# Kernel optimization log

Hardware: AMD Instinct MI355X
Metric: run time of the kernel (lower is better)

The kernel has to match this reference:

```python
import jax, jax.numpy as jnp
import numpy as np

WEIGHT = 1.0
TEMPERATURE = 1.0
POWER = 2.0
NEG_FILL = -1e9
EPS = 1e-8


def _cos_sim_matrix(x):
    # row-normalize then GEMM: equivalent to pairwise F.cosine_similarity
    norms = jnp.linalg.norm(x, axis=-1, keepdims=True)
    xn = x / jnp.maximum(norms, EPS)
    return xn @ xn.T  # [N, N]


def setup_inputs() -> dict:
    key = jax.random.key(0)
    k1, k2 = jax.random.split(key)
    model_output = jax.random.normal(k1, (8192, 512), dtype=jnp.float32)
    targets = jax.random.normal(k2, (8192, 768), dtype=jnp.float32)
    return {"model_output": model_output, "targets": targets}


def reference(model_output, targets):
    N = model_output.shape[0]
    eye = jnp.eye(N, dtype=bool)

    sim_o = jnp.where(eye, NEG_FILL, _cos_sim_matrix(model_output))
    sim_t = jnp.where(eye, NEG_FILL, _cos_sim_matrix(targets))

    student_log_probs = jax.nn.log_softmax(sim_o / TEMPERATURE, axis=-1)
    teacher_probs = jax.nn.softmax(sim_t / TEMPERATURE, axis=-1)

    weights = jax.lax.stop_gradient(teacher_probs ** POWER)

    # torch F.kl_div(input=log_p_student, target=p_teacher, reduction='none')
    # = where(target > 0, target * (log(target) - input), 0)
    tp_safe = jnp.where(teacher_probs > 0, teacher_probs, 1.0)
    kl = jnp.where(teacher_probs > 0,
                   teacher_probs * (jnp.log(tp_safe) - student_log_probs),
                   0.0)

    loss = jnp.mean(weights * kl)
    return WEIGHT * loss
```

## Files before the change

### kernel.cpp

```cpp
#include <hip/hip_runtime.h>

#define N    8192
#define DT   768
#define DO   512
#define BM   128
#define BN   128
#define TI   (N / BM)
#define TJ   (N / BN)
#define NTILE (TI * (TI + 1) / 2)
#define NSLOT (2 * TJ)
#define PL    ((size_t)NSLOT * N)

typedef __attribute__((ext_vector_type(8))) short   short8;
typedef __attribute__((ext_vector_type(4))) float   floatx4;

struct alignas(8) us4 { unsigned short x[4]; };

__device__ inline unsigned short f2bf(float x) {
    union { float f; unsigned int u; } v; v.f = x;
    unsigned int r = v.u + 0x7fffu + ((v.u >> 16) & 1u);
    return (unsigned short)(r >> 16);
}
__device__ inline float bf2f(unsigned short u) {
    union { unsigned int u; float f; } v; v.u = ((unsigned int)u) << 16;
    return v.f;
}

__device__ inline void gl2lds16(const unsigned short* g, unsigned short* l) {
    __builtin_amdgcn_global_load_lds(
        (const __attribute__((address_space(1))) unsigned int*)(const void*)g,
        (__attribute__((address_space(3))) unsigned int*)(void*)l,
        16, 0, 0);
}

template <int D>
__device__ inline void stage_tile(const unsigned short* __restrict__ Xi,
                                  const unsigned short* __restrict__ Xj,
                                  unsigned short* sA, unsigned short* sB,
                                  int i0, int j0, int k, int t) {
    #pragma unroll
    for (int h = 0; h < 2; ++h) {
        const int idx = t + h * 256;
        const int r   = idx >> 2;
        const int cs  = ((idx & 3) ^ ((r >> 1) & 3)) << 3;
        gl2lds16(Xi + (size_t)(i0 + r) * D + k + cs, &sA[idx * 8]);
        gl2lds16(Xj + (size_t)(j0 + r) * D + k + cs, &sB[idx * 8]);
    }
}

__global__ void norm_kernel(const float* __restrict__ Tg,
                            const float* __restrict__ Mo,
                            unsigned short* __restrict__ Xt,
                            unsigned short* __restrict__ Xo,
                            float* __restrict__ zero_me) {
    if (blockIdx.x == 0 && threadIdx.x == 0) zero_me[0] = 0.0f;
    int bid = blockIdx.x;
    const float* X; unsigned short* Xn; int D;
    if (bid < N / 4) { X = Tg; Xn = Xt; D = DT; }
    else             { bid -= N / 4; X = Mo; Xn = Xo; D = DO; }
    const int row  = bid * 4 + (threadIdx.x >> 6);
    const int lane = threadIdx.x & 63;
    const float* xr = X + (size_t)row * D;
    float ss = 0.0f;
    for (int c = lane * 4; c < D; c += 256) {
        const floatx4 v = *(const floatx4*)(xr + c);
        ss += v[0] * v[0] + v[1] * v[1] + v[2] * v[2] + v[3] * v[3];
    }
    #pragma unroll
    for (int m = 32; m >= 1; m >>= 1) ss += __shfl_xor(ss, m);
    const float scale = 1.0f / fmaxf(sqrtf(ss), 1e-8f);
    unsigned short* outr = Xn + (size_t)row * D;
    for (int c = lane * 4; c < D; c += 256) {
        const floatx4 v = *(const floatx4*)(xr + c);
        us4 o;
        #pragma unroll
        for (int j = 0; j < 4; ++j) o.x[j] = f2bf(v[j] * scale);
        *(us4*)(outr + c) = o;
    }
}

__launch_bounds__(256, 3)
__global__ void fused_kernel(const unsigned short* __restrict__ Xt,
                             const unsigned short* __restrict__ Xo,
                             float* __restrict__ partials) {
    __shared__ unsigned short sA[BM * 32];
    __shared__ unsigned short sB[BN * 32];
    __shared__ unsigned short sW[64 * 256];

    const int t    = threadIdx.x;
    const int lane = t & 63;
    const int w    = t >> 6;
    const int wm   = w >> 1, wn = w & 1;
    const int lr   = lane & 15, lg = lane >> 4;
    const int swz  = (lr >> 1) & 3;

    const int swb = (blockIdx.x & 7) * (NTILE / 8) + (blockIdx.x >> 3);
    int rem = swb, ti = 0;
    while (rem >= TI - ti) { rem -= TI - ti; ++ti; }
    const int tj = ti + rem;
    const bool offdiag = (ti != tj);
    const int i0 = ti * BM, j0 = tj * BN;

    floatx4 acc[4][4];
    #pragma unroll
    for (int a = 0; a < 4; ++a)
        #pragma unroll
        for (int b = 0; b < 4; ++b)
            acc[a][b] = (floatx4){0.0f, 0.0f, 0.0f, 0.0f};

    for (int k = 0; k < DT; k += 32) {
        stage_tile<DT>(Xt, Xt, sA, sB, i0, j0, k, t);
        asm volatile("s_waitcnt vmcnt(0)" ::: "memory");
        __syncthreads();
        short8 af[4], bf[4];
        #pragma unroll
        for (int mi = 0; mi < 4; ++mi)
            af[mi] = *(const short8*)&sA[(wm * 64 + mi * 16 + lr) * 32 + ((lg ^ swz) << 3)];
        #pragma unroll
        for (int ni = 0; ni < 4; ++ni)
            bf[ni] = *(const short8*)&sB[(wn * 64 + ni * 16 + lr) * 32 + ((lg ^ swz) << 3)];
        #pragma unroll
        for (int mi = 0; mi < 4; ++mi)
            #pragma unroll
            for (int ni = 0; ni < 4; ++ni)
                acc[mi][ni] = __builtin_amdgcn_mfma_f32_16x16x32_bf16(
                    af[mi], bf[ni], acc[mi][ni], 0, 0, 0);
        __syncthreads();
    }

    {
        float czt[4], cvv[4], cua[4];
        #pragma unroll
        for (int ni = 0; ni < 4; ++ni) { czt[ni] = 0.0f; cvv[ni] = 0.0f; cua[ni] = 0.0f; }
        #pragma unroll
        for (int mi = 0; mi < 4; ++mi) {
            #pragma unroll
            for (int r = 0; r < 4; ++r) {
                const int row = wm * 64 + mi * 16 + lg * 4 + r;
                const int gi  = i0 + row;
                float zt = 0.0f, vv = 0.0f, ua = 0.0f;
                #pragma unroll
                for (int ni = 0; ni < 4; ++ni) {
                    const int gj = j0 + wn * 64 + ni * 16 + lr;
                    const float a = acc[mi][ni][r];
                    float ea = __expf(a - 1.0f);
                    if (gi == gj) ea = 0.0f;
                    const float e3 = ea * ea * ea;
                    zt += ea; vv += e3; ua += e3 * a;
                    czt[ni] += ea; cvv[ni] += e3; cua[ni] += e3 * a;
                    sW[(mi * 16 + ni * 4 + r) * 256 + t] = f2bf(e3);
                }
                #pragma unroll
                for (int m = 8; m >= 1; m >>= 1) {
                    zt += __shfl_xor(zt, m);
                    vv += __shfl_xor(vv, m);
                    ua += __shfl_xor(ua, m);
                }
                if (lr == 0) {
                    const size_t base = (size_t)(tj * 2 + wn) * N + gi;
                    partials[0 * PL + base] = zt;
                    partials[1 * PL + base] = vv;
                    partials[2 * PL + base] = ua;
                }
            }
        }
        if (offdiag) {
            #pragma unroll
            for (int ni = 0; ni < 4; ++ni) {
                #pragma unroll
                for (int m = 16; m <= 32; m <<= 1) {
                    czt[ni] += __shfl_xor(czt[ni], m);
                    cvv[ni] += __shfl_xor(cvv[ni], m);
                    cua[ni] += __shfl_xor(cua[ni], m);
                }
            }
            if (lg == 0) {
                #pragma unroll
                for (int ni = 0; ni < 4; ++ni) {
                    const int gj = j0 + wn * 64 + ni * 16 + lr;
                    const size_t base = (size_t)(ti * 2 + wm) * N + gj;
                    partials[0 * PL + base] = czt[ni];
                    partials[1 * PL + base] = cvv[ni];
                    partials[2 * PL + base] = cua[ni];
                }
            }
        }
    }

    #pragma unroll
    for (int a = 0; a < 4; ++a)
        #pragma unroll
        for (int b = 0; b < 4; ++b)
            acc[a][b] = (floatx4){0.0f, 0.0f, 0.0f, 0.0f};

    for (int k = 0; k < DO; k += 32) {
        stage_tile<DO>(Xo, Xo, sA, sB, i0, j0, k, t);
        asm volatile("s_waitcnt vmcnt(0)" ::: "memory");
        __syncthreads();
        short8 af[4], bf[4];
        #pragma unroll
        for (int mi = 0; mi < 4; ++mi)
            af[mi] = *(const short8*)&sA[(wm * 64 + mi * 16 + lr) * 32 + ((lg ^ swz) << 3)];
        #pragma unroll
        for (int ni = 0; ni < 4; ++ni)
            bf[ni] = *(const short8*)&sB[(wn * 64 + ni * 16 + lr) * 32 + ((lg ^ swz) << 3)];
        #pragma unroll
        for (int mi = 0; mi < 4; ++mi)
            #pragma unroll
            for (int ni = 0; ni < 4; ++ni)
                acc[mi][ni] = __builtin_amdgcn_mfma_f32_16x16x32_bf16(
                    af[mi], bf[ni], acc[mi][ni], 0, 0, 0);
        __syncthreads();
    }

    {
        float czo[4], cwb[4];
        #pragma unroll
        for (int ni = 0; ni < 4; ++ni) { czo[ni] = 0.0f; cwb[ni] = 0.0f; }
        #pragma unroll
        for (int mi = 0; mi < 4; ++mi) {
            #pragma unroll
            for (int r = 0; r < 4; ++r) {
                const int row = wm * 64 + mi * 16 + lg * 4 + r;
                const int gi  = i0 + row;
                float zo = 0.0f, wb = 0.0f;
                #pragma unroll
                for (int ni = 0; ni < 4; ++ni) {
                    const int gj = j0 + wn * 64 + ni * 16 + lr;
                    const float b = acc[mi][ni][r];
                    float eb = __expf(b - 1.0f);
                    if (gi == gj) eb = 0.0f;
                    const float wgt = bf2f(sW[(mi * 16 + ni * 4 + r) * 256 + t]);
                    zo += eb; wb += wgt * b;
                    czo[ni] += eb; cwb[ni] += wgt * b;
                }
                #pragma unroll
                for (int m = 8; m >= 1; m >>= 1) {
                    zo += __shfl_xor(zo, m);
                    wb += __shfl_xor(wb, m);
                }
                if (lr == 0) {
                    const size_t base = (size_t)(tj * 2 + wn) * N + gi;
                    partials[3 * PL + base] = zo;
                    partials[4 * PL + base] = wb;
                }
            }
        }
        if (offdiag) {
            #pragma unroll
            for (int ni = 0; ni < 4; ++ni) {
                #pragma unroll
                for (int m = 16; m <= 32; m <<= 1) {
                    czo[ni] += __shfl_xor(czo[ni], m);
                    cwb[ni] += __shfl_xor(cwb[ni], m);
                }
            }
            if (lg == 0) {
                #pragma unroll
                for (int ni = 0; ni < 4; ++ni) {
                    const int gj = j0 + wn * 64 + ni * 16 + lr;
                    const size_t base = (size_t)(ti * 2 + wm) * N + gj;
                    partials[3 * PL + base] = czo[ni];
                    partials[4 * PL + base] = cwb[ni];
                }
            }
        }
    }
}

__global__ void reduce_kernel(const float* __restrict__ partials,
                              float* __restrict__ out) {
    const int i = blockIdx.x * 256 + threadIdx.x;
    float zt = 0.0f, vv = 0.0f, ua = 0.0f, zo = 0.0f, wb = 0.0f;
    for (int jb = 0; jb < NSLOT; ++jb) {
        const size_t base = (size_t)jb * N + i;
        zt += partials[0 * PL + base];
        vv += partials[1 * PL + base];
        ua += partials[2 * PL + base];
        zo += partials[3 * PL + base];
        wb += partials[4 * PL + base];
    }
    float li = (ua - wb + vv * __logf(zo / zt)) / (zt * zt * zt);
    #pragma unroll
    for (int m = 32; m >= 1; m >>= 1) li += __shfl_xor(li, m);
    __shared__ float wsh[4];
    const int w = threadIdx.x >> 6;
    if ((threadIdx.x & 63) == 0) wsh[w] = li;
    __syncthreads();
    if (threadIdx.x == 0) {
        const float s = (wsh[0] + wsh[1] + wsh[2] + wsh[3]) *
                        (1.0f / ((float)N * (float)N));
        atomicAdd(out, s);
    }
}

extern "C" void kernel_launch(void* const* d_in, const int* in_sizes, int n_in,
                              void* d_out, int out_size, void* d_ws, size_t ws_size,
                              hipStream_t stream) {
    (void)in_sizes; (void)n_in; (void)out_size; (void)ws_size;
    const float* mo = (const float*)d_in[0];
    const float* tg = (const float*)d_in[1];
    float* out = (float*)d_out;

    char* ws = (char*)d_ws;
    unsigned short* Xt = (unsigned short*)ws;
    unsigned short* Xo = (unsigned short*)(ws + (size_t)N * DT * 2);
    float* partials    = (float*)(ws + (size_t)N * DT * 2 + (size_t)N * DO * 2);

    norm_kernel<<<2 * (N / 4), 256, 0, stream>>>(tg, mo, Xt, Xo, out);
    fused_kernel<<<NTILE, 256, 0, stream>>>(Xt, Xo, partials);
    reduce_kernel<<<N / 256, 256, 0, stream>>>(partials, out);
}
```

Measured before the change: 305.5 us.

## Double-buffer LDS tiles, keep teacher weights in registers, widen reduce parallelism

The GEMM K-loops now use two LDS buffers, so the next k-slice is prefetched while MFMAs run on the current one, with one barrier per step. The prefetch chains from the teacher GEMM into the first slice of the student GEMM. The bf16 teacher weights e3 are packed into 32 registers instead of a 32 KB LDS array. This cuts LDS use but raises register pressure, which could hurt occupancy at launch bounds of 3. The reduce kernel splits the slot loop across 4 waves per 64 rows and launches 4x more blocks to expose more memory parallelism.

```diff
diff --git a/kernel.cpp b/kernel.cpp
--- a/kernel.cpp
+++ b/kernel.cpp
@@ -10,6 +10,8 @@
 #define NTILE (TI * (TI + 1) / 2)
 #define NSLOT (2 * TJ)
 #define PL    ((size_t)NSLOT * N)
+#define NKT   (DT / 32)
+#define NKO   (DO / 32)
 
 typedef __attribute__((ext_vector_type(8))) short   short8;
 typedef __attribute__((ext_vector_type(4))) float   floatx4;
@@ -36,16 +38,41 @@
 template <int D>
 __device__ inline void stage_tile(const unsigned short* __restrict__ Xi,
                                   const unsigned short* __restrict__ Xj,
-                                  unsigned short* sA, unsigned short* sB,
+                                  unsigned short* sAb, unsigned short* sBb,
                                   int i0, int j0, int k, int t) {
     #pragma unroll
     for (int h = 0; h < 2; ++h) {
         const int idx = t + h * 256;
         const int r   = idx >> 2;
         const int cs  = ((idx & 3) ^ ((r >> 1) & 3)) << 3;
-        gl2lds16(Xi + (size_t)(i0 + r) * D + k + cs, &sA[idx * 8]);
-        gl2lds16(Xj + (size_t)(j0 + r) * D + k + cs, &sB[idx * 8]);
-    }
+        gl2lds16(Xi + (size_t)(i0 + r) * D + k + cs, &sAb[idx * 8]);
+        gl2lds16(Xj + (size_t)(j0 + r) * D + k + cs, &sBb[idx * 8]);
+    }
+}
+
+__device__ inline void mfma_step(const unsigned short* __restrict__ sAb,
+                                 const unsigned short* __restrict__ sBb,
+                                 floatx4 (&acc)[4][4],
+                                 int wm, int wn, int lr, int lgx) {
+    short8 af[4], bf[4];
+    #pragma unroll
+    for (int mi = 0; mi < 4; ++mi)
+        af[mi] = *(const short8*)&sAb[(wm * 64 + mi * 16 + lr) * 32 + (lgx << 3)];
+    #pragma unroll
+    for (int ni = 0; ni < 4; ++ni)
+        bf[ni] = *(const short8*)&sBb[(wn * 64 + ni * 16 + lr) * 32 + (lgx << 3)];
+    #pragma unroll
+    for (int mi = 0; mi < 4; ++mi)
+        #pragma unroll
+        for (int ni = 0; ni < 4; ++ni)
+            acc[mi][ni] = __builtin_amdgcn_mfma_f32_16x16x32_bf16(
+                af[mi], bf[ni], acc[mi][ni], 0, 0, 0);
+}
+
+__device__ inline void drain_barrier() {
+    asm volatile("s_waitcnt vmcnt(0)" ::: "memory");
+    __builtin_amdgcn_s_barrier();
+    asm volatile("" ::: "memory");
 }
 
 __global__ void norm_kernel(const float* __restrict__ Tg,
@@ -83,16 +110,15 @@
 __global__ void fused_kernel(const unsigned short* __restrict__ Xt,
                              const unsigned short* __restrict__ Xo,
                              float* __restrict__ partials) {
-    __shared__ unsigned short sA[BM * 32];
-    __shared__ unsigned short sB[BN * 32];
-    __shared__ unsigned short sW[64 * 256];
+    __shared__ unsigned short sA[2][BM * 32];
+    __shared__ unsigned short sB[2][BN * 32];
 
     const int t    = threadIdx.x;
     const int lane = t & 63;
     const int w    = t >> 6;
     const int wm   = w >> 1, wn = w & 1;
     const int lr   = lane & 15, lg = lane >> 4;
-    const int swz  = (lr >> 1) & 3;
+    const int lgx  = lg ^ ((lr >> 1) & 3);
 
     const int swb = (blockIdx.x & 7) * (NTILE / 8) + (blockIdx.x >> 3);
     int rem = swb, ti = 0;
@@ -101,6 +127,7 @@
     const bool offdiag = (ti != tj);
     const int i0 = ti * BM, j0 = tj * BN;
 
+    unsigned int w3p[32];
     floatx4 acc[4][4];
     #pragma unroll
     for (int a = 0; a < 4; ++a)
@@ -108,24 +135,15 @@
         for (int b = 0; b < 4; ++b)
             acc[a][b] = (floatx4){0.0f, 0.0f, 0.0f, 0.0f};
 
-    for (int k = 0; k < DT; k += 32) {
-        stage_tile<DT>(Xt, Xt, sA, sB, i0, j0, k, t);
-        asm volatile("s_waitcnt vmcnt(0)" ::: "memory");
-        __syncthreads();
-        short8 af[4], bf[4];
-        #pragma unroll
-        for (int mi = 0; mi < 4; ++mi)
-            af[mi] = *(const short8*)&sA[(wm * 64 + mi * 16 + lr) * 32 + ((lg ^ swz) << 3)];
-        #pragma unroll
-        for (int ni = 0; ni < 4; ++ni)
-            bf[ni] = *(const short8*)&sB[(wn * 64 + ni * 16 + lr) * 32 + ((lg ^ swz) << 3)];
-        #pragma unroll
-        for (int mi = 0; mi < 4; ++mi)
-            #pragma unroll
-            for (int ni = 0; ni < 4; ++ni)
-                acc[mi][ni] = __builtin_amdgcn_mfma_f32_16x16x32_bf16(
-                    af[mi], bf[ni], acc[mi][ni], 0, 0, 0);
-        __syncthreads();
+    stage_tile<DT>(Xt, Xt, sA[0], sB[0], i0, j0, 0, t);
+    drain_barrier();
+
+    for (int kt = 0; kt < NKT; ++kt) {
+        const int cur = kt & 1, nxt = cur ^ 1;
+        if (kt + 1 < NKT) stage_tile<DT>(Xt, Xt, sA[nxt], sB[nxt], i0, j0, (kt + 1) * 32, t);
+        else              stage_tile<DO>(Xo, Xo, sA[nxt], sB[nxt], i0, j0, 0, t);
+        mfma_step(sA[cur], sB[cur], acc, wm, wn, lr, lgx);
+        drain_barrier();
     }
 
     {
@@ -148,7 +166,10 @@
                     const float e3 = ea * ea * ea;
                     zt += ea; vv += e3; ua += e3 * a;
                     czt[ni] += ea; cvv[ni] += e3; cua[ni] += e3 * a;
-                    sW[(mi * 16 + ni * 4 + r) * 256 + t] = f2bf(e3);
+                    const int idx = mi * 16 + ni * 4 + r;
+                    const unsigned short h = f2bf(e3);
+                    if (idx & 1) w3p[idx >> 1] |= ((unsigned int)h) << 16;
+                    else         w3p[idx >> 1]  = (unsigned int)h;
                 }
                 #pragma unroll
                 for (int m = 8; m >= 1; m >>= 1) {
@@ -193,24 +214,11 @@
         for (int b = 0; b < 4; ++b)
             acc[a][b] = (floatx4){0.0f, 0.0f, 0.0f, 0.0f};
 
-    for (int k = 0; k < DO; k += 32) {
-        stage_tile<DO>(Xo, Xo, sA, sB, i0, j0, k, t);
-        asm volatile("s_waitcnt vmcnt(0)" ::: "memory");
-        __syncthreads();
-        short8 af[4], bf[4];
-        #pragma unroll
-        for (int mi = 0; mi < 4; ++mi)
-            af[mi] = *(const short8*)&sA[(wm * 64 + mi * 16 + lr) * 32 + ((lg ^ swz) << 3)];
-        #pragma unroll
-        for (int ni = 0; ni < 4; ++ni)
-            bf[ni] = *(const short8*)&sB[(wn * 64 + ni * 16 + lr) * 32 + ((lg ^ swz) << 3)];
-        #pragma unroll
-        for (int mi = 0; mi < 4; ++mi)
-            #pragma unroll
-            for (int ni = 0; ni < 4; ++ni)
-                acc[mi][ni] = __builtin_amdgcn_mfma_f32_16x16x32_bf16(
-                    af[mi], bf[ni], acc[mi][ni], 0, 0, 0);
-        __syncthreads();
+    for (int ko = 0; ko < NKO; ++ko) {
+        const int cur = ko & 1, nxt = cur ^ 1;
+        if (ko + 1 < NKO) stage_tile<DO>(Xo, Xo, sA[nxt], sB[nxt], i0, j0, (ko + 1) * 32, t);
+        mfma_step(sA[cur], sB[cur], acc, wm, wn, lr, lgx);
+        if (ko + 1 < NKO) drain_barrier();
     }
 
     {
@@ -230,7 +238,10 @@
                     const float b = acc[mi][ni][r];
                     float eb = __expf(b - 1.0f);
                     if (gi == gj) eb = 0.0f;
-                    const float wgt = bf2f(sW[(mi * 16 + ni * 4 + r) * 256 + t]);
+                    const int idx = mi * 16 + ni * 4 + r;
+                    const unsigned int pw = w3p[idx >> 1];
+                    const float wgt = bf2f((unsigned short)((idx & 1) ? (pw >> 16)
+                                                                      : (pw & 0xffffu)));
                     zo += eb; wb += wgt * b;
                     czo[ni] += eb; cwb[ni] += wgt * b;
                 }
@@ -270,27 +281,30 @@
 
 __global__ void reduce_kernel(const float* __restrict__ partials,
                               float* __restrict__ out) {
-    const int i = blockIdx.x * 256 + threadIdx.x;
-    float zt = 0.0f, vv = 0.0f, ua = 0.0f, zo = 0.0f, wb = 0.0f;
-    for (int jb = 0; jb < NSLOT; ++jb) {
+    __shared__ float sh[5][256];
+    const int t    = threadIdx.x;
+    const int lane = t & 63;
+    const int g    = t >> 6;
+    const int i    = blockIdx.x * 64 + lane;
+    float s[5] = {0.0f, 0.0f, 0.0f, 0.0f, 0.0f};
+    for (int jb = g * (NSLOT / 4); jb < (g + 1) * (NSLOT / 4); ++jb) {
         const size_t base = (size_t)jb * N + i;
-        zt += partials[0 * PL + base];
-        vv += partials[1 * PL + base];
-        ua += partials[2 * PL + base];
-        zo += partials[3 * PL + base];
-        wb += partials[4 * PL + base];
-    }
-    float li = (ua - wb + vv * __logf(zo / zt)) / (zt * zt * zt);
-    #pragma unroll
-    for (int m = 32; m >= 1; m >>= 1) li += __shfl_xor(li, m);
-    __shared__ float wsh[4];
-    const int w = threadIdx.x >> 6;
-    if ((threadIdx.x & 63) == 0) wsh[w] = li;
+        #pragma unroll
+        for (int p = 0; p < 5; ++p) s[p] += partials[p * PL + base];
+    }
+    #pragma unroll
+    for (int p = 0; p < 5; ++p) sh[p][t] = s[p];
     __syncthreads();
-    if (threadIdx.x == 0) {
-        const float s = (wsh[0] + wsh[1] + wsh[2] + wsh[3]) *
-                        (1.0f / ((float)N * (float)N));
-        atomicAdd(out, s);
+    if (g == 0) {
+        float v[5];
+        #pragma unroll
+        for (int p = 0; p < 5; ++p)
+            v[p] = sh[p][lane] + sh[p][64 + lane] + sh[p][128 + lane] + sh[p][192 + lane];
+        float li = (v[2] - v[4] + v[1] * __logf(v[3] / v[0])) / (v[0] * v[0] * v[0]);
+        #pragma unroll
+        for (int m = 32; m >= 1; m >>= 1) li += __shfl_xor(li, m);
+        if (lane == 0)
+            atomicAdd(out, li * (1.0f / ((float)N * (float)N)));
     }
 }
 
@@ -309,5 +323,5 @@
 
     norm_kernel<<<2 * (N / 4), 256, 0, stream>>>(tg, mo, Xt, Xo, out);
     fused_kernel<<<NTILE, 256, 0, stream>>>(Xt, Xo, partials);
-    reduce_kernel<<<N / 256, 256, 0, stream>>>(partials, out);
-}
+    reduce_kernel<<<N / 64, 256, 0, stream>>>(partials, out);
+}
```

Result: slower. 377.2 us (+23.5%).
